# Optimization experiments

Hardware: AMD Instinct MI355X
Metric: run time of the kernel (lower is better)

Reference implementation:

```python
import jax, jax.numpy as jnp
import numpy as np

SCALE = 1.0 / np.sqrt(64.0)  # 1/sqrt(d), d = head_dim


def setup_inputs() -> dict:
    key = jax.random.key(0)
    kq, kk, kv = jax.random.split(key, 3)
    shape = (32, 2048, 64)  # [batch*num_heads, seq_len, head_dim]
    return {
        "queries": jax.random.normal(kq, shape, dtype=jnp.float32),
        "keys": jax.random.normal(kk, shape, dtype=jnp.float32),
        "values": jax.random.normal(kv, shape, dtype=jnp.float32),
    }


def reference(queries, keys, values):
    # scores = Q K^T / sqrt(d)   -> [n, q_len, kv_len]
    scores = jnp.einsum("nqd,nkd->nqk", queries, keys) * SCALE
    # masked_softmax with mask=None == plain softmax over last axis
    attn = jax.nn.softmax(scores, axis=-1)
    # dropout rate 0 / inference -> identity
    return jnp.einsum("nqk,nkd->nqd", attn, values)
```

## Files before the change

kernel.cpp:

```cpp
#include <hip/hip_runtime.h>
#include <hip/hip_bf16.h>

#define SEQ   2048
#define HDIM  64
#define KVT   64
#define NT    (SEQ / KVT)
#define M0    12.0f
#define QSC   0.18033688011112042f

typedef float f32x16 __attribute__((ext_vector_type(16)));
typedef short bf16x8 __attribute__((ext_vector_type(8)));
typedef short bf16x4 __attribute__((ext_vector_type(4)));

#define MFMA32(a, b, c) __builtin_amdgcn_mfma_f32_32x32x16_bf16(a, b, c, 0, 0, 0)

static __device__ __forceinline__ unsigned tobf(float x) {
    unsigned u = __builtin_bit_cast(unsigned, x);
    u += 0x7fff + ((u >> 16) & 1);
    return u >> 16;
}
static __device__ __forceinline__ unsigned pk2(float lo, float hi) {
    return (tobf(hi) << 16) | tobf(lo);
}
static __device__ __forceinline__ unsigned pkrn(float lo, float hi) {
    __hip_bfloat162 h = __float22bfloat162_rn(make_float2(lo, hi));
    unsigned r;
    __builtin_memcpy(&r, &h, sizeof(r));
    return r;
}

static __device__ __forceinline__ void gll16(const void* g, void* l) {
    __builtin_amdgcn_global_load_lds(
        (const __attribute__((address_space(1))) void*)g,
        (__attribute__((address_space(3))) void*)l, 16, 0, 0);
}

__global__ __launch_bounds__(256) void attn_prep(
    const float* __restrict__ K, const float* __restrict__ V,
    unsigned short* __restrict__ Kx, unsigned short* __restrict__ Vx)
{
    __shared__ unsigned short tile[64 * 64];
    const int bid = blockIdx.x;
    const int tid = threadIdx.x;
    if (bid < 4096) {
        const int id  = bid * 256 + tid;
        const int h   = id >> 15;
        const int key = (id >> 4) & 2047;
        const int f   = id & 15;
        const float4 kv = *(const float4*)(K + ((size_t)h * SEQ + key) * HDIM + f * 4);
        unsigned* dst = (unsigned*)(Kx + ((size_t)h * SEQ + key) * HDIM + ((f ^ (key & 15)) << 2));
        dst[0] = pk2(kv.x, kv.y);
        dst[1] = pk2(kv.z, kv.w);
    } else {
        const int b = bid - 4096;
        const int h = b >> 5, t = b & 31;
        const float* vb = V + ((size_t)h * SEQ + t * 64) * HDIM;
#pragma unroll
        for (int i = 0; i < 4; ++i) {
            const int idx = tid + i * 256;
            const int key = idx >> 4, f = idx & 15;
            float4 vv = *(const float4*)(vb + key * HDIM + f * 4);
            unsigned* d = (unsigned*)&tile[key * 64 + f * 4];
            d[0] = pk2(vv.x, vv.y);
            d[1] = pk2(vv.z, vv.w);
        }
        __syncthreads();
        unsigned short* vxb = Vx + ((size_t)h * SEQ + t * 64) * HDIM;
        const int dim = tid & 63;
#pragma unroll
        for (int j = 0; j < 4; ++j) {
            const int kb = (tid >> 6) + j * 4;
            const unsigned short s0 = tile[(kb * 4 + 0) * 64 + dim];
            const unsigned short s1 = tile[(kb * 4 + 1) * 64 + dim];
            const unsigned short s2 = tile[(kb * 4 + 2) * 64 + dim];
            const unsigned short s3 = tile[(kb * 4 + 3) * 64 + dim];
            unsigned* d = (unsigned*)&vxb[dim * 64 + ((kb ^ (dim & 15)) << 2)];
            d[0] = (unsigned)s0 | ((unsigned)s1 << 16);
            d[1] = (unsigned)s2 | ((unsigned)s3 << 16);
        }
    }
}

#define KBUF 8192

__global__ __launch_bounds__(256, 2) void attn_v5(
    const float* __restrict__ Q, const unsigned short* __restrict__ Kx,
    const unsigned short* __restrict__ Vx, float* __restrict__ O)
{
    __shared__ __align__(16) short Ks[2][KVT * HDIM];
    __shared__ __align__(16) short Vf[2][KVT * HDIM];
    __shared__ float Linv[128];

    const int tid  = threadIdx.x;
    const int lane = tid & 63;
    const int wid  = tid >> 6;
    const int n31  = lane & 31;
    const int hi   = lane >> 5;
    const int m15  = n31 & 15;

    const int id = blockIdx.x;
    const int n  = (id & 7) + 8 * (id >> 7);
    const int qt = (id >> 3) & 15;
    const int qb = qt * 128 + wid * 32;

    const float* Qb = Q + (size_t)n * SEQ * HDIM;
    const char* kg = (const char*)(Kx + (size_t)n * SEQ * HDIM);
    const char* vg = (const char*)(Vx + (size_t)n * SEQ * HDIM);

    int offKa_[4], offKb_[4];
#pragma unroll
    for (int c = 0; c < 4; ++c) {
        const int ba = (4 * c + 2 * hi) ^ m15;
        offKa_[c] = n31 * 128 + (ba << 3);
        offKb_[c] = n31 * 128 + ((ba ^ 1) << 3);
    }
    int offV_[2][4];
#pragma unroll
    for (int h = 0; h < 2; ++h)
#pragma unroll
    for (int i = 0; i < 4; ++i)
        offV_[h][i] = n31 * 128 + ((((8 * h + hi + 2 * i) ^ m15)) << 3);

    bf16x8 qf[4];
#pragma unroll
    for (int c = 0; c < 4; ++c) {
        const float* qp = Qb + (size_t)(qb + n31) * HDIM + c * 16 + hi * 8;
        float4 a = *(const float4*)qp;
        float4 b = *(const float4*)(qp + 4);
        union { unsigned w[4]; bf16x8 v; } u;
        u.w[0] = pkrn(a.x * QSC, a.y * QSC);
        u.w[1] = pkrn(a.z * QSC, a.w * QSC);
        u.w[2] = pkrn(b.x * QSC, b.y * QSC);
        u.w[3] = pkrn(b.z * QSC, b.w * QSC);
        qf[c] = u.v;
    }

    f32x16 NEGM;
#pragma unroll
    for (int r = 0; r < 16; ++r) NEGM[r] = -M0;

    f32x16 o0, o1;
#pragma unroll
    for (int r = 0; r < 16; ++r) { o0[r] = 0.f; o1[r] = 0.f; }
    float lac = 0.f;

    const int soff = wid * 1024 + lane * 16;

#define STAGE(GOFF, BUF)                                                         \
    {                                                                            \
        _Pragma("unroll")                                                        \
        for (int i = 0; i < 2; ++i) {                                            \
            gll16(kg + (GOFF) + soff + i * 4096,                                 \
                  (char*)Ks + (BUF) * KBUF + wid * 1024 + i * 4096);             \
            gll16(vg + (GOFF) + soff + i * 4096,                                 \
                  (char*)Vf + (BUF) * KBUF + wid * 1024 + i * 4096);             \
        }                                                                        \
    }

#define COMPUTE(BUF)                                                             \
    {                                                                            \
        _Pragma("unroll")                                                        \
        for (int h = 0; h < 2; ++h) {                                            \
            f32x16 s;                                                            \
            __builtin_amdgcn_s_setprio(1);                                       \
            {                                                                    \
                bf16x4 lo0 = *(const bf16x4*)((char*)Ks + (BUF) * KBUF + h * 4096 + offKa_[0]); \
                bf16x4 hh0 = *(const bf16x4*)((char*)Ks + (BUF) * KBUF + h * 4096 + offKb_[0]); \
                s = MFMA32(__builtin_shufflevector(lo0, hh0, 0, 1, 2, 3, 4, 5, 6, 7), qf[0], NEGM); \
            }                                                                    \
            _Pragma("unroll")                                                    \
            for (int c = 1; c < 4; ++c) {                                        \
                bf16x4 lo = *(const bf16x4*)((char*)Ks + (BUF) * KBUF + h * 4096 + offKa_[c]); \
                bf16x4 hh = *(const bf16x4*)((char*)Ks + (BUF) * KBUF + h * 4096 + offKb_[c]); \
                s = MFMA32(__builtin_shufflevector(lo, hh, 0, 1, 2, 3, 4, 5, 6, 7), qf[c], s); \
            }                                                                    \
            __builtin_amdgcn_s_setprio(0);                                       \
            float p[16];                                                         \
            _Pragma("unroll")                                                    \
            for (int r = 0; r < 16; ++r) p[r] = __builtin_amdgcn_exp2f(s[r]);    \
            {                                                                    \
                float a0 = (p[0] + p[1]) + (p[2] + p[3]);                        \
                float a1 = (p[4] + p[5]) + (p[6] + p[7]);                        \
                float a2 = (p[8] + p[9]) + (p[10] + p[11]);                      \
                float a3 = (p[12] + p[13]) + (p[14] + p[15]);                    \
                lac += (a0 + a1) + (a2 + a3);                                    \
            }                                                                    \
            union { unsigned w[4]; bf16x8 v; } pa1, pa2;                         \
            _Pragma("unroll")                                                    \
            for (int j = 0; j < 4; ++j) {                                        \
                pa1.w[j] = pkrn(p[2 * j], p[2 * j + 1]);                         \
                pa2.w[j] = pkrn(p[8 + 2 * j], p[8 + 2 * j + 1]);                 \
            }                                                                    \
            __builtin_amdgcn_s_setprio(1);                                       \
            _Pragma("unroll")                                                    \
            for (int dh = 0; dh < 2; ++dh) {                                     \
                bf16x4 u0 = *(const bf16x4*)((char*)Vf + (BUF) * KBUF + dh * 4096 + offV_[h][0]); \
                bf16x4 u1 = *(const bf16x4*)((char*)Vf + (BUF) * KBUF + dh * 4096 + offV_[h][1]); \
                bf16x4 u2 = *(const bf16x4*)((char*)Vf + (BUF) * KBUF + dh * 4096 + offV_[h][2]); \
                bf16x4 u3 = *(const bf16x4*)((char*)Vf + (BUF) * KBUF + dh * 4096 + offV_[h][3]); \
                bf16x8 v1 = __builtin_shufflevector(u0, u1, 0, 1, 2, 3, 4, 5, 6, 7); \
                bf16x8 v2 = __builtin_shufflevector(u2, u3, 0, 1, 2, 3, 4, 5, 6, 7); \
                if (dh == 0) { o0 = MFMA32(pa1.v, v1, o0); o0 = MFMA32(pa2.v, v2, o0); } \
                else         { o1 = MFMA32(pa1.v, v1, o1); o1 = MFMA32(pa2.v, v2, o1); } \
            }                                                                    \
            __builtin_amdgcn_s_setprio(0);                                       \
        }                                                                        \
    }

    STAGE(0, 0);
    asm volatile("s_waitcnt vmcnt(0)");
    __syncthreads();

    for (int t = 0; t < NT; t += 2) {
        const int g = t * 8192;
        STAGE(g + 8192, 1);
        COMPUTE(0);
        asm volatile("s_waitcnt vmcnt(0)");
        __syncthreads();
        if (t + 2 < NT) STAGE(g + 16384, 0);
        COMPUTE(1);
        asm volatile("s_waitcnt vmcnt(0)");
        __syncthreads();
    }

    float l = lac + __shfl_xor(lac, 32);
    if (hi == 0) Linv[wid * 32 + n31] = 1.f / l;
    __syncthreads();

    const size_t obase = ((size_t)n * SEQ + qb) * HDIM + n31;
#pragma unroll
    for (int r = 0; r < 16; ++r) {
        const int qrow = (r & 3) + 8 * (r >> 2) + 4 * hi;
        const float inv = Linv[wid * 32 + qrow];
        O[obase + (size_t)qrow * HDIM]      = o0[r] * inv;
        O[obase + (size_t)qrow * HDIM + 32] = o1[r] * inv;
    }
#undef STAGE
#undef COMPUTE
}

__global__ __launch_bounds__(256, 2) void attn_v3(
    const float* __restrict__ Q, const float* __restrict__ K,
    const float* __restrict__ V, float* __restrict__ O)
{
    __shared__ __align__(16) short Ks[2][KVT * HDIM];
    __shared__ __align__(16) short Vf[2][KVT * HDIM];
    __shared__ float Linv[128];

    const int tid  = threadIdx.x;
    const int lane = tid & 63;
    const int wid  = tid >> 6;
    const int n31  = lane & 31;
    const int hi   = lane >> 5;
    const int m15  = n31 & 15;

    const int id = blockIdx.x;
    const int n  = (id & 7) + 8 * (id >> 7);
    const int qt = (id >> 3) & 15;
    const int qb = qt * 128 + wid * 32;

    const float* Qb = Q + (size_t)n * SEQ * HDIM;
    const float* Kb = K + (size_t)n * SEQ * HDIM;
    const float* Vb = V + (size_t)n * SEQ * HDIM;

    const int sk_k0 = tid >> 4;
    const int sk_f  = tid & 15;
    const int sv_k  = tid & 63;
    const int sv_d0 = tid >> 6;

    bf16x8 qf[4];
#pragma unroll
    for (int c = 0; c < 4; ++c) {
        const float* qp = Qb + (size_t)(qb + n31) * HDIM + c * 16 + hi * 8;
        float4 a = *(const float4*)qp;
        float4 b = *(const float4*)(qp + 4);
        union { unsigned w[4]; bf16x8 v; } u;
        u.w[0] = pk2(a.x * QSC, a.y * QSC);
        u.w[1] = pk2(a.z * QSC, a.w * QSC);
        u.w[2] = pk2(b.x * QSC, b.y * QSC);
        u.w[3] = pk2(b.z * QSC, b.w * QSC);
        qf[c] = u.v;
    }

    f32x16 o0, o1;
#pragma unroll
    for (int r = 0; r < 16; ++r) { o0[r] = 0.f; o1[r] = 0.f; }
    float lac = 0.f;

    float4 kreg[4], vreg[4];

#define LOADT(T)                                                                \
    {                                                                           \
        const float* kp_ = Kb + (size_t)(T) * KVT * HDIM;                       \
        const float* vp_ = Vb + (size_t)(T) * KVT * HDIM;                       \
        _Pragma("unroll")                                                       \
        for (int i = 0; i < 4; ++i) {                                           \
            kreg[i] = *(const float4*)(kp_ + (sk_k0 + i * 16) * HDIM + sk_f * 4);\
            vreg[i] = *(const float4*)(vp_ + sv_k * HDIM + (sv_d0 + i * 4) * 4);\
        }                                                                       \
    }

#define WRITET(B)                                                               \
    {                                                                           \
        _Pragma("unroll")                                                       \
        for (int i = 0; i < 4; ++i) {                                           \
            const int k_ = sk_k0 + i * 16;                                      \
            union { unsigned w[2]; bf16x4 v; } u_;                              \
            u_.w[0] = pk2(kreg[i].x, kreg[i].y);                                \
            u_.w[1] = pk2(kreg[i].z, kreg[i].w);                                \
            *(bf16x4*)&Ks[B][k_ * 64 + ((sk_f ^ (k_ & 15)) << 2)] = u_.v;       \
            const int dq_ = sv_d0 + i * 4;                                      \
            const unsigned w0_ = pk2(vreg[i].x, vreg[i].y);                     \
            const unsigned w1_ = pk2(vreg[i].z, vreg[i].w);                     \
            _Pragma("unroll")                                                   \
            for (int r = 0; r < 4; ++r) {                                       \
                const int row_ = dq_ * 4 + r;                                   \
                const short val_ = (r == 0) ? (short)(w0_ & 0xffff)             \
                                 : (r == 1) ? (short)(w0_ >> 16)                \
                                 : (r == 2) ? (short)(w1_ & 0xffff)             \
                                            : (short)(w1_ >> 16);               \
                Vf[B][row_ * 64 + ((((sv_k >> 2) ^ (row_ & 15)) << 2) | (sv_k & 3))] = val_; \
            }                                                                   \
        }                                                                       \
    }

    LOADT(0);
    WRITET(0);
    __syncthreads();

    for (int t = 0; t < NT; ++t) {
        const int cur = t & 1;
        if (t + 1 < NT) LOADT(t + 1);

#pragma unroll
        for (int h = 0; h < 2; ++h) {
            const int key = h * 32 + n31;
            const short* Kp = &Ks[cur][key * 64];
            const int kx = key & 15;

            f32x16 s;
#pragma unroll
            for (int r = 0; r < 16; ++r) s[r] = -M0;

            __builtin_amdgcn_s_setprio(1);
#pragma unroll
            for (int c = 0; c < 4; ++c) {
                const int ba = 4 * c + 2 * hi;
                bf16x4 lo = *(const bf16x4*)&Kp[((ba    ) ^ kx) << 2];
                bf16x4 hh = *(const bf16x4*)&Kp[((ba + 1) ^ kx) << 2];
                bf16x8 kf = __builtin_shufflevector(lo, hh, 0, 1, 2, 3, 4, 5, 6, 7);
                s = MFMA32(kf, qf[c], s);
            }
            __builtin_amdgcn_s_setprio(0);

            float p[16];
#pragma unroll
            for (int r = 0; r < 16; ++r) p[r] = __builtin_amdgcn_exp2f(s[r]);
            {
                float a0 = (p[0] + p[1]) + (p[2] + p[3]);
                float a1 = (p[4] + p[5]) + (p[6] + p[7]);
                float a2 = (p[8] + p[9]) + (p[10] + p[11]);
                float a3 = (p[12] + p[13]) + (p[14] + p[15]);
                lac += (a0 + a1) + (a2 + a3);
            }

            union { unsigned w[4]; bf16x8 v; } pa1, pa2;
#pragma unroll
            for (int j = 0; j < 4; ++j) {
                pa1.w[j] = pk2(p[2 * j], p[2 * j + 1]);
                pa2.w[j] = pk2(p[8 + 2 * j], p[8 + 2 * j + 1]);
            }

            __builtin_amdgcn_s_setprio(1);
#pragma unroll
            for (int dh = 0; dh < 2; ++dh) {
                const short* Vp = &Vf[cur][(dh * 32 + n31) * 64];
                const int b0 = 8 * h + hi;
                bf16x4 u0 = *(const bf16x4*)&Vp[((b0    ) ^ m15) << 2];
                bf16x4 u1 = *(const bf16x4*)&Vp[((b0 + 2) ^ m15) << 2];
                bf16x4 u2 = *(const bf16x4*)&Vp[((b0 + 4) ^ m15) << 2];
                bf16x4 u3 = *(const bf16x4*)&Vp[((b0 + 6) ^ m15) << 2];
                bf16x8 v1 = __builtin_shufflevector(u0, u1, 0, 1, 2, 3, 4, 5, 6, 7);
                bf16x8 v2 = __builtin_shufflevector(u2, u3, 0, 1, 2, 3, 4, 5, 6, 7);
                if (dh == 0) { o0 = MFMA32(pa1.v, v1, o0); o0 = MFMA32(pa2.v, v2, o0); }
                else         { o1 = MFMA32(pa1.v, v1, o1); o1 = MFMA32(pa2.v, v2, o1); }
            }
            __builtin_amdgcn_s_setprio(0);
        }

        if (t + 1 < NT) WRITET((t + 1) & 1);
        __syncthreads();
    }

    float l = lac + __shfl_xor(lac, 32);
    if (hi == 0) Linv[wid * 32 + n31] = 1.f / l;
    __syncthreads();

    const size_t obase = ((size_t)n * SEQ + qb) * HDIM + n31;
#pragma unroll
    for (int r = 0; r < 16; ++r) {
        const int qrow = (r & 3) + 8 * (r >> 2) + 4 * hi;
        const float inv = Linv[wid * 32 + qrow];
        O[obase + (size_t)qrow * HDIM]      = o0[r] * inv;
        O[obase + (size_t)qrow * HDIM + 32] = o1[r] * inv;
    }
}

extern "C" void kernel_launch(void* const* d_in, const int* in_sizes, int n_in,
                              void* d_out, int out_size, void* d_ws, size_t ws_size,
                              hipStream_t stream) {
    const float* Q = (const float*)d_in[0];
    const float* K = (const float*)d_in[1];
    const float* V = (const float*)d_in[2];
    float* O = (float*)d_out;

    const size_t elems = (size_t)32 * SEQ * HDIM;
    const int nblk = (SEQ / 128) * 32;

    if (ws_size >= elems * 2 * 2) {
        unsigned short* Kx = (unsigned short*)d_ws;
        unsigned short* Vx = Kx + elems;
        attn_prep<<<4096 + 1024, 256, 0, stream>>>(K, V, Kx, Vx);
        attn_v5<<<nblk, 256, 0, stream>>>(Q, Kx, Vx, O);
    } else {
        attn_v3<<<nblk, 256, 0, stream>>>(Q, K, V, O);
    }
}
```

Measured before the change: 67.75 us.

## Split KV sequence across two wave groups per block and merge partial outputs

The attention kernel now launches 512 threads per block. Two halves of four waves each process disjoint halves of the key/value sequence for the same 128 query rows, using separate double-buffered shared memory regions. At the end, the second half writes its partial output accumulators and row sums to shared memory, and the first half adds them in, normalizes and stores. This doubles the waves available to hide latency and halves the serial KV loop per wave. The cost is more shared memory per block, a merge step and possibly lower block occupancy.

```diff
diff --git a/kernel.cpp b/kernel.cpp
--- a/kernel.cpp
+++ b/kernel.cpp
@@ -4,7 +4,6 @@
 #define SEQ   2048
 #define HDIM  64
 #define KVT   64
-#define NT    (SEQ / KVT)
 #define M0    12.0f
 #define QSC   0.18033688011112042f
 
@@ -82,18 +81,22 @@
 }
 
 #define KBUF 8192
-
-__global__ __launch_bounds__(256, 2) void attn_v5(
+#define HSTR 16384
+
+__global__ __launch_bounds__(512, 2) void attn_v6(
     const float* __restrict__ Q, const unsigned short* __restrict__ Kx,
     const unsigned short* __restrict__ Vx, float* __restrict__ O)
 {
-    __shared__ __align__(16) short Ks[2][KVT * HDIM];
-    __shared__ __align__(16) short Vf[2][KVT * HDIM];
+    __shared__ __align__(16) short Ks[2][2][KVT * HDIM];
+    __shared__ __align__(16) short Vf[2][2][KVT * HDIM];
+    __shared__ float L2[128];
     __shared__ float Linv[128];
 
     const int tid  = threadIdx.x;
     const int lane = tid & 63;
     const int wid  = tid >> 6;
+    const int qw   = wid & 3;
+    const int half = wid >> 2;
     const int n31  = lane & 31;
     const int hi   = lane >> 5;
     const int m15  = n31 & 15;
@@ -101,11 +104,13 @@
     const int id = blockIdx.x;
     const int n  = (id & 7) + 8 * (id >> 7);
     const int qt = (id >> 3) & 15;
-    const int qb = qt * 128 + wid * 32;
+    const int qb = qt * 128 + qw * 32;
 
     const float* Qb = Q + (size_t)n * SEQ * HDIM;
-    const char* kg = (const char*)(Kx + (size_t)n * SEQ * HDIM);
-    const char* vg = (const char*)(Vx + (size_t)n * SEQ * HDIM);
+    const char* kg = (const char*)(Kx + (size_t)n * SEQ * HDIM) + (size_t)half * 131072;
+    const char* vg = (const char*)(Vx + (size_t)n * SEQ * HDIM) + (size_t)half * 131072;
+    char* KsH = (char*)Ks + half * HSTR;
+    char* VfH = (char*)Vf + half * HSTR;
 
     int offKa_[4], offKb_[4];
 #pragma unroll
@@ -144,16 +149,16 @@
     for (int r = 0; r < 16; ++r) { o0[r] = 0.f; o1[r] = 0.f; }
     float lac = 0.f;
 
-    const int soff = wid * 1024 + lane * 16;
+    const int soff = qw * 1024 + lane * 16;
 
 #define STAGE(GOFF, BUF)                                                         \
     {                                                                            \
         _Pragma("unroll")                                                        \
         for (int i = 0; i < 2; ++i) {                                            \
             gll16(kg + (GOFF) + soff + i * 4096,                                 \
-                  (char*)Ks + (BUF) * KBUF + wid * 1024 + i * 4096);             \
+                  KsH + (BUF) * KBUF + qw * 1024 + i * 4096);                    \
             gll16(vg + (GOFF) + soff + i * 4096,                                 \
-                  (char*)Vf + (BUF) * KBUF + wid * 1024 + i * 4096);             \
+                  VfH + (BUF) * KBUF + qw * 1024 + i * 4096);                    \
         }                                                                        \
     }
 
@@ -164,14 +169,14 @@
             f32x16 s;                                                            \
             __builtin_amdgcn_s_setprio(1);                                       \
             {                                                                    \
-                bf16x4 lo0 = *(const bf16x4*)((char*)Ks + (BUF) * KBUF + h * 4096 + offKa_[0]); \
-                bf16x4 hh0 = *(const bf16x4*)((char*)Ks + (BUF) * KBUF + h * 4096 + offKb_[0]); \
+                bf16x4 lo0 = *(const bf16x4*)(KsH + (BUF) * KBUF + h * 4096 + offKa_[0]); \
+                bf16x4 hh0 = *(const bf16x4*)(KsH + (BUF) * KBUF + h * 4096 + offKb_[0]); \
                 s = MFMA32(__builtin_shufflevector(lo0, hh0, 0, 1, 2, 3, 4, 5, 6, 7), qf[0], NEGM); \
             }                                                                    \
             _Pragma("unroll")                                                    \
             for (int c = 1; c < 4; ++c) {                                        \
-                bf16x4 lo = *(const bf16x4*)((char*)Ks + (BUF) * KBUF + h * 4096 + offKa_[c]); \
-                bf16x4 hh = *(const bf16x4*)((char*)Ks + (BUF) * KBUF + h * 4096 + offKb_[c]); \
+                bf16x4 lo = *(const bf16x4*)(KsH + (BUF) * KBUF + h * 4096 + offKa_[c]); \
+                bf16x4 hh = *(const bf16x4*)(KsH + (BUF) * KBUF + h * 4096 + offKb_[c]); \
                 s = MFMA32(__builtin_shufflevector(lo, hh, 0, 1, 2, 3, 4, 5, 6, 7), qf[c], s); \
             }                                                                    \
             __builtin_amdgcn_s_setprio(0);                                       \
@@ -194,10 +199,10 @@
             __builtin_amdgcn_s_setprio(1);                                       \
             _Pragma("unroll")                                                    \
             for (int dh = 0; dh < 2; ++dh) {                                     \
-                bf16x4 u0 = *(const bf16x4*)((char*)Vf + (BUF) * KBUF + dh * 4096 + offV_[h][0]); \
-                bf16x4 u1 = *(const bf16x4*)((char*)Vf + (BUF) * KBUF + dh * 4096 + offV_[h][1]); \
-                bf16x4 u2 = *(const bf16x4*)((char*)Vf + (BUF) * KBUF + dh * 4096 + offV_[h][2]); \
-                bf16x4 u3 = *(const bf16x4*)((char*)Vf + (BUF) * KBUF + dh * 4096 + offV_[h][3]); \
+                bf16x4 u0 = *(const bf16x4*)(VfH + (BUF) * KBUF + dh * 4096 + offV_[h][0]); \
+                bf16x4 u1 = *(const bf16x4*)(VfH + (BUF) * KBUF + dh * 4096 + offV_[h][1]); \
+                bf16x4 u2 = *(const bf16x4*)(VfH + (BUF) * KBUF + dh * 4096 + offV_[h][2]); \
+                bf16x4 u3 = *(const bf16x4*)(VfH + (BUF) * KBUF + dh * 4096 + offV_[h][3]); \
                 bf16x8 v1 = __builtin_shufflevector(u0, u1, 0, 1, 2, 3, 4, 5, 6, 7); \
                 bf16x8 v2 = __builtin_shufflevector(u2, u3, 0, 1, 2, 3, 4, 5, 6, 7); \
                 if (dh == 0) { o0 = MFMA32(pa1.v, v1, o0); o0 = MFMA32(pa2.v, v2, o0); } \
@@ -211,29 +216,48 @@
     asm volatile("s_waitcnt vmcnt(0)");
     __syncthreads();
 
-    for (int t = 0; t < NT; t += 2) {
+    for (int t = 0; t < 16; t += 2) {
         const int g = t * 8192;
         STAGE(g + 8192, 1);
         COMPUTE(0);
         asm volatile("s_waitcnt vmcnt(0)");
         __syncthreads();
-        if (t + 2 < NT) STAGE(g + 16384, 0);
+        if (t + 2 < 16) STAGE(g + 16384, 0);
         COMPUTE(1);
         asm volatile("s_waitcnt vmcnt(0)");
         __syncthreads();
     }
 
     float l = lac + __shfl_xor(lac, 32);
-    if (hi == 0) Linv[wid * 32 + n31] = 1.f / l;
+
+    if (half == 1) {
+        if (hi == 0) L2[qw * 32 + n31] = l;
+        float* ob = (float*)((char*)Ks + qw * 8192) + lane * 32;
+        *(f32x16*)(ob)      = o0;
+        *(f32x16*)(ob + 16) = o1;
+    }
     __syncthreads();
 
-    const size_t obase = ((size_t)n * SEQ + qb) * HDIM + n31;
-#pragma unroll
-    for (int r = 0; r < 16; ++r) {
-        const int qrow = (r & 3) + 8 * (r >> 2) + 4 * hi;
-        const float inv = Linv[wid * 32 + qrow];
-        O[obase + (size_t)qrow * HDIM]      = o0[r] * inv;
-        O[obase + (size_t)qrow * HDIM + 32] = o1[r] * inv;
+    if (half == 0) {
+        const float* pb = (const float*)((char*)Ks + qw * 8192) + lane * 32;
+        f32x16 p0 = *(const f32x16*)(pb);
+        f32x16 p1 = *(const f32x16*)(pb + 16);
+#pragma unroll
+        for (int r = 0; r < 16; ++r) { o0[r] += p0[r]; o1[r] += p1[r]; }
+        l += L2[qw * 32 + n31];
+        if (hi == 0) Linv[qw * 32 + n31] = 1.f / l;
+    }
+    __syncthreads();
+
+    if (half == 0) {
+        const size_t obase = ((size_t)n * SEQ + qb) * HDIM + n31;
+#pragma unroll
+        for (int r = 0; r < 16; ++r) {
+            const int qrow = (r & 3) + 8 * (r >> 2) + 4 * hi;
+            const float inv = Linv[qw * 32 + qrow];
+            O[obase + (size_t)qrow * HDIM]      = o0[r] * inv;
+            O[obase + (size_t)qrow * HDIM + 32] = o1[r] * inv;
+        }
     }
 #undef STAGE
 #undef COMPUTE
@@ -243,9 +267,9 @@
     const float* __restrict__ Q, const float* __restrict__ K,
     const float* __restrict__ V, float* __restrict__ O)
 {
-    __shared__ __align__(16) short Ks[2][KVT * HDIM];
-    __shared__ __align__(16) short Vf[2][KVT * HDIM];
-    __shared__ float Linv[128];
+    __shared__ __align__(16) short Ksf[2][KVT * HDIM];
+    __shared__ __align__(16) short Vff[2][KVT * HDIM];
+    __shared__ float LinvF[128];
 
     const int tid  = threadIdx.x;
     const int lane = tid & 63;
@@ -308,7 +332,7 @@
             union { unsigned w[2]; bf16x4 v; } u_;                              \
             u_.w[0] = pk2(kreg[i].x, kreg[i].y);                                \
             u_.w[1] = pk2(kreg[i].z, kreg[i].w);                                \
-            *(bf16x4*)&Ks[B][k_ * 64 + ((sk_f ^ (k_ & 15)) << 2)] = u_.v;       \
+            *(bf16x4*)&Ksf[B][k_ * 64 + ((sk_f ^ (k_ & 15)) << 2)] = u_.v;      \
             const int dq_ = sv_d0 + i * 4;                                      \
             const unsigned w0_ = pk2(vreg[i].x, vreg[i].y);                     \
             const unsigned w1_ = pk2(vreg[i].z, vreg[i].w);                     \
@@ -319,7 +343,7 @@
                                  : (r == 1) ? (short)(w0_ >> 16)                \
                                  : (r == 2) ? (short)(w1_ & 0xffff)             \
                                             : (short)(w1_ >> 16);               \
-                Vf[B][row_ * 64 + ((((sv_k >> 2) ^ (row_ & 15)) << 2) | (sv_k & 3))] = val_; \
+                Vff[B][row_ * 64 + ((((sv_k >> 2) ^ (row_ & 15)) << 2) | (sv_k & 3))] = val_; \
             }                                                                   \
         }                                                                       \
     }
@@ -328,14 +352,14 @@
     WRITET(0);
     __syncthreads();
 
-    for (int t = 0; t < NT; ++t) {
+    for (int t = 0; t < SEQ / KVT; ++t) {
         const int cur = t & 1;
-        if (t + 1 < NT) LOADT(t + 1);
+        if (t + 1 < SEQ / KVT) LOADT(t + 1);
 
 #pragma unroll
         for (int h = 0; h < 2; ++h) {
             const int key = h * 32 + n31;
-            const short* Kp = &Ks[cur][key * 64];
+            const short* Kp = &Ksf[cur][key * 64];
             const int kx = key & 15;
 
             f32x16 s;
@@ -374,7 +398,7 @@
             __builtin_amdgcn_s_setprio(1);
 #pragma unroll
             for (int dh = 0; dh < 2; ++dh) {
-                const short* Vp = &Vf[cur][(dh * 32 + n31) * 64];
+                const short* Vp = &Vff[cur][(dh * 32 + n31) * 64];
                 const int b0 = 8 * h + hi;
                 bf16x4 u0 = *(const bf16x4*)&Vp[((b0    ) ^ m15) << 2];
                 bf16x4 u1 = *(const bf16x4*)&Vp[((b0 + 2) ^ m15) << 2];
@@ -388,19 +412,19 @@
             __builtin_amdgcn_s_setprio(0);
         }
 
-        if (t + 1 < NT) WRITET((t + 1) & 1);
+        if (t + 1 < SEQ / KVT) WRITET((t + 1) & 1);
         __syncthreads();
     }
 
     float l = lac + __shfl_xor(lac, 32);
-    if (hi == 0) Linv[wid * 32 + n31] = 1.f / l;
+    if (hi == 0) LinvF[wid * 32 + n31] = 1.f / l;
     __syncthreads();
 
     const size_t obase = ((size_t)n * SEQ + qb) * HDIM + n31;
 #pragma unroll
     for (int r = 0; r < 16; ++r) {
         const int qrow = (r & 3) + 8 * (r >> 2) + 4 * hi;
-        const float inv = Linv[wid * 32 + qrow];
+        const float inv = LinvF[wid * 32 + qrow];
         O[obase + (size_t)qrow * HDIM]      = o0[r] * inv;
         O[obase + (size_t)qrow * HDIM + 32] = o1[r] * inv;
     }
@@ -421,7 +445,7 @@
         unsigned short* Kx = (unsigned short*)d_ws;
         unsigned short* Vx = Kx + elems;
         attn_prep<<<4096 + 1024, 256, 0, stream>>>(K, V, Kx, Vx);
-        attn_v5<<<nblk, 256, 0, stream>>>(Q, Kx, Vx, O);
+        attn_v6<<<nblk, 512, 0, stream>>>(Q, Kx, Vx, O);
     } else {
         attn_v3<<<nblk, 256, 0, stream>>>(Q, K, V, O);
     }
```

Result: slower. 74.46 us (+9.9%).

## Split KV sequence across two blocks per query tile and add combine kernel

Applied to the files above, without the earlier changes.

Splits the key/value sequence into two halves, each processed by a separate block (1024 blocks, launch bounds raised to 4 per CU), writing unnormalized partial outputs in bf16 and row sums to workspace. A new combine kernel sums the partials and normalizes. This aims to raise occupancy and parallelism, at the cost of extra global traffic, an extra kernel launch, and bf16 rounding of partials. The small-workspace fallback now also writes to workspace.

```diff
diff --git a/kernel.cpp b/kernel.cpp
--- a/kernel.cpp
+++ b/kernel.cpp
@@ -5,6 +5,7 @@
 #define HDIM  64
 #define KVT   64
 #define NT    (SEQ / KVT)
+#define HT    16
 #define M0    12.0f
 #define QSC   0.18033688011112042f
 
@@ -27,6 +28,9 @@
     unsigned r;
     __builtin_memcpy(&r, &h, sizeof(r));
     return r;
+}
+static __device__ __forceinline__ float bf2f(unsigned short u) {
+    return __builtin_bit_cast(float, ((unsigned)u) << 16);
 }
 
 static __device__ __forceinline__ void gll16(const void* g, void* l) {
@@ -83,13 +87,13 @@
 
 #define KBUF 8192
 
-__global__ __launch_bounds__(256, 2) void attn_v5(
+__global__ __launch_bounds__(256, 4) void attn_v7(
     const float* __restrict__ Q, const unsigned short* __restrict__ Kx,
-    const unsigned short* __restrict__ Vx, float* __restrict__ O)
+    const unsigned short* __restrict__ Vx,
+    unsigned short* __restrict__ Pp, float* __restrict__ Lp)
 {
     __shared__ __align__(16) short Ks[2][KVT * HDIM];
     __shared__ __align__(16) short Vf[2][KVT * HDIM];
-    __shared__ float Linv[128];
 
     const int tid  = threadIdx.x;
     const int lane = tid & 63;
@@ -98,14 +102,16 @@
     const int hi   = lane >> 5;
     const int m15  = n31 & 15;
 
-    const int id = blockIdx.x;
-    const int n  = (id & 7) + 8 * (id >> 7);
-    const int qt = (id >> 3) & 15;
+    const int id    = blockIdx.x;
+    const int id9   = id & 511;
+    const int split = id >> 9;
+    const int n  = (id9 & 7) + 8 * (id9 >> 7);
+    const int qt = (id9 >> 3) & 15;
     const int qb = qt * 128 + wid * 32;
 
     const float* Qb = Q + (size_t)n * SEQ * HDIM;
-    const char* kg = (const char*)(Kx + (size_t)n * SEQ * HDIM);
-    const char* vg = (const char*)(Vx + (size_t)n * SEQ * HDIM);
+    const char* kg = (const char*)(Kx + (size_t)n * SEQ * HDIM) + (size_t)split * (HT * KBUF);
+    const char* vg = (const char*)(Vx + (size_t)n * SEQ * HDIM) + (size_t)split * (HT * KBUF);
 
     int offKa_[4], offKb_[4];
 #pragma unroll
@@ -211,6 +217,178 @@
     asm volatile("s_waitcnt vmcnt(0)");
     __syncthreads();
 
+    for (int t = 0; t < HT; t += 2) {
+        const int g = t * 8192;
+        STAGE(g + 8192, 1);
+        COMPUTE(0);
+        asm volatile("s_waitcnt vmcnt(0)");
+        __syncthreads();
+        if (t + 2 < HT) STAGE(g + 16384, 0);
+        COMPUTE(1);
+        asm volatile("s_waitcnt vmcnt(0)");
+        __syncthreads();
+    }
+
+    float l = lac + __shfl_xor(lac, 32);
+    if (hi == 0) Lp[split * 65536 + n * SEQ + qb + n31] = l;
+
+    unsigned short* pb = Pp + (size_t)split * 4194304
+                       + ((size_t)n * SEQ + qb) * HDIM + n31;
+#pragma unroll
+    for (int r = 0; r < 16; ++r) {
+        const int qrow = (r & 3) + 8 * (r >> 2) + 4 * hi;
+        pb[(size_t)qrow * HDIM]      = (unsigned short)tobf(o0[r]);
+        pb[(size_t)qrow * HDIM + 32] = (unsigned short)tobf(o1[r]);
+    }
+#undef STAGE
+#undef COMPUTE
+}
+
+__global__ __launch_bounds__(256) void attn_comb(
+    const unsigned short* __restrict__ Pp, const float* __restrict__ Lp,
+    float* __restrict__ O)
+{
+    const int f = blockIdx.x * 256 + threadIdx.x;
+    const int qidx = f >> 4;
+    const float inv = 1.f / (Lp[qidx] + Lp[65536 + qidx]);
+    const ushort4 a = *(const ushort4*)(Pp + (size_t)f * 4);
+    const ushort4 b = *(const ushort4*)(Pp + 4194304 + (size_t)f * 4);
+    float4 o;
+    o.x = (bf2f(a.x) + bf2f(b.x)) * inv;
+    o.y = (bf2f(a.y) + bf2f(b.y)) * inv;
+    o.z = (bf2f(a.z) + bf2f(b.z)) * inv;
+    o.w = (bf2f(a.w) + bf2f(b.w)) * inv;
+    reinterpret_cast<float4*>(O)[f] = o;
+}
+
+__global__ __launch_bounds__(256, 2) void attn_v5(
+    const float* __restrict__ Q, const unsigned short* __restrict__ Kx,
+    const unsigned short* __restrict__ Vx, float* __restrict__ O)
+{
+    __shared__ __align__(16) short Ks[2][KVT * HDIM];
+    __shared__ __align__(16) short Vf[2][KVT * HDIM];
+    __shared__ float Linv[128];
+
+    const int tid  = threadIdx.x;
+    const int lane = tid & 63;
+    const int wid  = tid >> 6;
+    const int n31  = lane & 31;
+    const int hi   = lane >> 5;
+    const int m15  = n31 & 15;
+
+    const int id = blockIdx.x;
+    const int n  = (id & 7) + 8 * (id >> 7);
+    const int qt = (id >> 3) & 15;
+    const int qb = qt * 128 + wid * 32;
+
+    const float* Qb = Q + (size_t)n * SEQ * HDIM;
+    const char* kg = (const char*)(Kx + (size_t)n * SEQ * HDIM);
+    const char* vg = (const char*)(Vx + (size_t)n * SEQ * HDIM);
+
+    int offKa_[4], offKb_[4];
+#pragma unroll
+    for (int c = 0; c < 4; ++c) {
+        const int ba = (4 * c + 2 * hi) ^ m15;
+        offKa_[c] = n31 * 128 + (ba << 3);
+        offKb_[c] = n31 * 128 + ((ba ^ 1) << 3);
+    }
+    int offV_[2][4];
+#pragma unroll
+    for (int h = 0; h < 2; ++h)
+#pragma unroll
+    for (int i = 0; i < 4; ++i)
+        offV_[h][i] = n31 * 128 + ((((8 * h + hi + 2 * i) ^ m15)) << 3);
+
+    bf16x8 qf[4];
+#pragma unroll
+    for (int c = 0; c < 4; ++c) {
+        const float* qp = Qb + (size_t)(qb + n31) * HDIM + c * 16 + hi * 8;
+        float4 a = *(const float4*)qp;
+        float4 b = *(const float4*)(qp + 4);
+        union { unsigned w[4]; bf16x8 v; } u;
+        u.w[0] = pkrn(a.x * QSC, a.y * QSC);
+        u.w[1] = pkrn(a.z * QSC, a.w * QSC);
+        u.w[2] = pkrn(b.x * QSC, b.y * QSC);
+        u.w[3] = pkrn(b.z * QSC, b.w * QSC);
+        qf[c] = u.v;
+    }
+
+    f32x16 NEGM;
+#pragma unroll
+    for (int r = 0; r < 16; ++r) NEGM[r] = -M0;
+
+    f32x16 o0, o1;
+#pragma unroll
+    for (int r = 0; r < 16; ++r) { o0[r] = 0.f; o1[r] = 0.f; }
+    float lac = 0.f;
+
+    const int soff = wid * 1024 + lane * 16;
+
+#define STAGE(GOFF, BUF)                                                         \
+    {                                                                            \
+        _Pragma("unroll")                                                        \
+        for (int i = 0; i < 2; ++i) {                                            \
+            gll16(kg + (GOFF) + soff + i * 4096,                                 \
+                  (char*)Ks + (BUF) * KBUF + wid * 1024 + i * 4096);             \
+            gll16(vg + (GOFF) + soff + i * 4096,                                 \
+                  (char*)Vf + (BUF) * KBUF + wid * 1024 + i * 4096);             \
+        }                                                                        \
+    }
+
+#define COMPUTE(BUF)                                                             \
+    {                                                                            \
+        _Pragma("unroll")                                                        \
+        for (int h = 0; h < 2; ++h) {                                            \
+            f32x16 s;                                                            \
+            __builtin_amdgcn_s_setprio(1);                                       \
+            {                                                                    \
+                bf16x4 lo0 = *(const bf16x4*)((char*)Ks + (BUF) * KBUF + h * 4096 + offKa_[0]); \
+                bf16x4 hh0 = *(const bf16x4*)((char*)Ks + (BUF) * KBUF + h * 4096 + offKb_[0]); \
+                s = MFMA32(__builtin_shufflevector(lo0, hh0, 0, 1, 2, 3, 4, 5, 6, 7), qf[0], NEGM); \
+            }                                                                    \
+            _Pragma("unroll")                                                    \
+            for (int c = 1; c < 4; ++c) {                                        \
+                bf16x4 lo = *(const bf16x4*)((char*)Ks + (BUF) * KBUF + h * 4096 + offKa_[c]); \
+                bf16x4 hh = *(const bf16x4*)((char*)Ks + (BUF) * KBUF + h * 4096 + offKb_[c]); \
+                s = MFMA32(__builtin_shufflevector(lo, hh, 0, 1, 2, 3, 4, 5, 6, 7), qf[c], s); \
+            }                                                                    \
+            __builtin_amdgcn_s_setprio(0);                                       \
+            float p[16];                                                         \
+            _Pragma("unroll")                                                    \
+            for (int r = 0; r < 16; ++r) p[r] = __builtin_amdgcn_exp2f(s[r]);    \
+            {                                                                    \
+                float a0 = (p[0] + p[1]) + (p[2] + p[3]);                        \
+                float a1 = (p[4] + p[5]) + (p[6] + p[7]);                        \
+                float a2 = (p[8] + p[9]) + (p[10] + p[11]);                      \
+                float a3 = (p[12] + p[13]) + (p[14] + p[15]);                    \
+                lac += (a0 + a1) + (a2 + a3);                                    \
+            }                                                                    \
+            union { unsigned w[4]; bf16x8 v; } pa1, pa2;                         \
+            _Pragma("unroll")                                                    \
+            for (int j = 0; j < 4; ++j) {                                        \
+                pa1.w[j] = pkrn(p[2 * j], p[2 * j + 1]);                         \
+                pa2.w[j] = pkrn(p[8 + 2 * j], p[8 + 2 * j + 1]);                 \
+            }                                                                    \
+            __builtin_amdgcn_s_setprio(1);                                       \
+            _Pragma("unroll")                                                    \
+            for (int dh = 0; dh < 2; ++dh) {                                     \
+                bf16x4 u0 = *(const bf16x4*)((char*)Vf + (BUF) * KBUF + dh * 4096 + offV_[h][0]); \
+                bf16x4 u1 = *(const bf16x4*)((char*)Vf + (BUF) * KBUF + dh * 4096 + offV_[h][1]); \
+                bf16x4 u2 = *(const bf16x4*)((char*)Vf + (BUF) * KBUF + dh * 4096 + offV_[h][2]); \
+                bf16x4 u3 = *(const bf16x4*)((char*)Vf + (BUF) * KBUF + dh * 4096 + offV_[h][3]); \
+                bf16x8 v1 = __builtin_shufflevector(u0, u1, 0, 1, 2, 3, 4, 5, 6, 7); \
+                bf16x8 v2 = __builtin_shufflevector(u2, u3, 0, 1, 2, 3, 4, 5, 6, 7); \
+                if (dh == 0) { o0 = MFMA32(pa1.v, v1, o0); o0 = MFMA32(pa2.v, v2, o0); } \
+                else         { o1 = MFMA32(pa1.v, v1, o1); o1 = MFMA32(pa2.v, v2, o1); } \
+            }                                                                    \
+            __builtin_amdgcn_s_setprio(0);                                       \
+        }                                                                        \
+    }
+
+    STAGE(0, 0);
+    asm volatile("s_waitcnt vmcnt(0)");
+    __syncthreads();
+
     for (int t = 0; t < NT; t += 2) {
         const int g = t * 8192;
         STAGE(g + 8192, 1);
@@ -239,173 +417,6 @@
 #undef COMPUTE
 }
 
-__global__ __launch_bounds__(256, 2) void attn_v3(
-    const float* __restrict__ Q, const float* __restrict__ K,
-    const float* __restrict__ V, float* __restrict__ O)
-{
-    __shared__ __align__(16) short Ks[2][KVT * HDIM];
-    __shared__ __align__(16) short Vf[2][KVT * HDIM];
-    __shared__ float Linv[128];
-
-    const int tid  = threadIdx.x;
-    const int lane = tid & 63;
-    const int wid  = tid >> 6;
-    const int n31  = lane & 31;
-    const int hi   = lane >> 5;
-    const int m15  = n31 & 15;
-
-    const int id = blockIdx.x;
-    const int n  = (id & 7) + 8 * (id >> 7);
-    const int qt = (id >> 3) & 15;
-    const int qb = qt * 128 + wid * 32;
-
-    const float* Qb = Q + (size_t)n * SEQ * HDIM;
-    const float* Kb = K + (size_t)n * SEQ * HDIM;
-    const float* Vb = V + (size_t)n * SEQ * HDIM;
-
-    const int sk_k0 = tid >> 4;
-    const int sk_f  = tid & 15;
-    const int sv_k  = tid & 63;
-    const int sv_d0 = tid >> 6;
-
-    bf16x8 qf[4];
-#pragma unroll
-    for (int c = 0; c < 4; ++c) {
-        const float* qp = Qb + (size_t)(qb + n31) * HDIM + c * 16 + hi * 8;
-        float4 a = *(const float4*)qp;
-        float4 b = *(const float4*)(qp + 4);
-        union { unsigned w[4]; bf16x8 v; } u;
-        u.w[0] = pk2(a.x * QSC, a.y * QSC);
-        u.w[1] = pk2(a.z * QSC, a.w * QSC);
-        u.w[2] = pk2(b.x * QSC, b.y * QSC);
-        u.w[3] = pk2(b.z * QSC, b.w * QSC);
-        qf[c] = u.v;
-    }
-
-    f32x16 o0, o1;
-#pragma unroll
-    for (int r = 0; r < 16; ++r) { o0[r] = 0.f; o1[r] = 0.f; }
-    float lac = 0.f;
-
-    float4 kreg[4], vreg[4];
-
-#define LOADT(T)                                                                \
-    {                                                                           \
-        const float* kp_ = Kb + (size_t)(T) * KVT * HDIM;                       \
-        const float* vp_ = Vb + (size_t)(T) * KVT * HDIM;                       \
-        _Pragma("unroll")                                                       \
-        for (int i = 0; i < 4; ++i) {                                           \
-            kreg[i] = *(const float4*)(kp_ + (sk_k0 + i * 16) * HDIM + sk_f * 4);\
-            vreg[i] = *(const float4*)(vp_ + sv_k * HDIM + (sv_d0 + i * 4) * 4);\
-        }                                                                       \
-    }
-
-#define WRITET(B)                                                               \
-    {                                                                           \
-        _Pragma("unroll")                                                       \
-        for (int i = 0; i < 4; ++i) {                                           \
-            const int k_ = sk_k0 + i * 16;                                      \
-            union { unsigned w[2]; bf16x4 v; } u_;                              \
-            u_.w[0] = pk2(kreg[i].x, kreg[i].y);                                \
-            u_.w[1] = pk2(kreg[i].z, kreg[i].w);                                \
-            *(bf16x4*)&Ks[B][k_ * 64 + ((sk_f ^ (k_ & 15)) << 2)] = u_.v;       \
-            const int dq_ = sv_d0 + i * 4;                                      \
-            const unsigned w0_ = pk2(vreg[i].x, vreg[i].y);                     \
-            const unsigned w1_ = pk2(vreg[i].z, vreg[i].w);                     \
-            _Pragma("unroll")                                                   \
-            for (int r = 0; r < 4; ++r) {                                       \
-                const int row_ = dq_ * 4 + r;                                   \
-                const short val_ = (r == 0) ? (short)(w0_ & 0xffff)             \
-                                 : (r == 1) ? (short)(w0_ >> 16)                \
-                                 : (r == 2) ? (short)(w1_ & 0xffff)             \
-                                            : (short)(w1_ >> 16);               \
-                Vf[B][row_ * 64 + ((((sv_k >> 2) ^ (row_ & 15)) << 2) | (sv_k & 3))] = val_; \
-            }                                                                   \
-        }                                                                       \
-    }
-
-    LOADT(0);
-    WRITET(0);
-    __syncthreads();
-
-    for (int t = 0; t < NT; ++t) {
-        const int cur = t & 1;
-        if (t + 1 < NT) LOADT(t + 1);
-
-#pragma unroll
-        for (int h = 0; h < 2; ++h) {
-            const int key = h * 32 + n31;
-            const short* Kp = &Ks[cur][key * 64];
-            const int kx = key & 15;
-
-            f32x16 s;
-#pragma unroll
-            for (int r = 0; r < 16; ++r) s[r] = -M0;
-
-            __builtin_amdgcn_s_setprio(1);
-#pragma unroll
-            for (int c = 0; c < 4; ++c) {
-                const int ba = 4 * c + 2 * hi;
-                bf16x4 lo = *(const bf16x4*)&Kp[((ba    ) ^ kx) << 2];
-                bf16x4 hh = *(const bf16x4*)&Kp[((ba + 1) ^ kx) << 2];
-                bf16x8 kf = __builtin_shufflevector(lo, hh, 0, 1, 2, 3, 4, 5, 6, 7);
-                s = MFMA32(kf, qf[c], s);
-            }
-            __builtin_amdgcn_s_setprio(0);
-
-            float p[16];
-#pragma unroll
-            for (int r = 0; r < 16; ++r) p[r] = __builtin_amdgcn_exp2f(s[r]);
-            {
-                float a0 = (p[0] + p[1]) + (p[2] + p[3]);
-                float a1 = (p[4] + p[5]) + (p[6] + p[7]);
-                float a2 = (p[8] + p[9]) + (p[10] + p[11]);
-                float a3 = (p[12] + p[13]) + (p[14] + p[15]);
-                lac += (a0 + a1) + (a2 + a3);
-            }
-
-            union { unsigned w[4]; bf16x8 v; } pa1, pa2;
-#pragma unroll
-            for (int j = 0; j < 4; ++j) {
-                pa1.w[j] = pk2(p[2 * j], p[2 * j + 1]);
-                pa2.w[j] = pk2(p[8 + 2 * j], p[8 + 2 * j + 1]);
-            }
-
-            __builtin_amdgcn_s_setprio(1);
-#pragma unroll
-            for (int dh = 0; dh < 2; ++dh) {
-                const short* Vp = &Vf[cur][(dh * 32 + n31) * 64];
-                const int b0 = 8 * h + hi;
-                bf16x4 u0 = *(const bf16x4*)&Vp[((b0    ) ^ m15) << 2];
-                bf16x4 u1 = *(const bf16x4*)&Vp[((b0 + 2) ^ m15) << 2];
-                bf16x4 u2 = *(const bf16x4*)&Vp[((b0 + 4) ^ m15) << 2];
-                bf16x4 u3 = *(const bf16x4*)&Vp[((b0 + 6) ^ m15) << 2];
-                bf16x8 v1 = __builtin_shufflevector(u0, u1, 0, 1, 2, 3, 4, 5, 6, 7);
-                bf16x8 v2 = __builtin_shufflevector(u2, u3, 0, 1, 2, 3, 4, 5, 6, 7);
-                if (dh == 0) { o0 = MFMA32(pa1.v, v1, o0); o0 = MFMA32(pa2.v, v2, o0); }
-                else         { o1 = MFMA32(pa1.v, v1, o1); o1 = MFMA32(pa2.v, v2, o1); }
-            }
-            __builtin_amdgcn_s_setprio(0);
-        }
-
-        if (t + 1 < NT) WRITET((t + 1) & 1);
-        __syncthreads();
-    }
-
-    float l = lac + __shfl_xor(lac, 32);
-    if (hi == 0) Linv[wid * 32 + n31] = 1.f / l;
-    __syncthreads();
-
-    const size_t obase = ((size_t)n * SEQ + qb) * HDIM + n31;
-#pragma unroll
-    for (int r = 0; r < 16; ++r) {
-        const int qrow = (r & 3) + 8 * (r >> 2) + 4 * hi;
-        const float inv = Linv[wid * 32 + qrow];
-        O[obase + (size_t)qrow * HDIM]      = o0[r] * inv;
-        O[obase + (size_t)qrow * HDIM + 32] = o1[r] * inv;
-    }
-}
-
 extern "C" void kernel_launch(void* const* d_in, const int* in_sizes, int n_in,
                               void* d_out, int out_size, void* d_ws, size_t ws_size,
                               hipStream_t stream) {
@@ -417,12 +428,21 @@
     const size_t elems = (size_t)32 * SEQ * HDIM;
     const int nblk = (SEQ / 128) * 32;
 
-    if (ws_size >= elems * 2 * 2) {
-        unsigned short* Kx = (unsigned short*)d_ws;
-        unsigned short* Vx = Kx + elems;
+    char* ws = (char*)d_ws;
+    unsigned short* Kx = (unsigned short*)ws;
+    unsigned short* Vx = (unsigned short*)(ws + 8388608);
+    unsigned short* Pp = (unsigned short*)(ws + 16777216);
+    float*          Lp = (float*)(ws + 33554432);
+
+    if (ws_size >= 34078720) {
+        attn_prep<<<4096 + 1024, 256, 0, stream>>>(K, V, Kx, Vx);
+        attn_v7<<<2 * nblk, 256, 0, stream>>>(Q, Kx, Vx, Pp, Lp);
+        attn_comb<<<4096, 256, 0, stream>>>(Pp, Lp, O);
+    } else if (ws_size >= elems * 2 * 2) {
         attn_prep<<<4096 + 1024, 256, 0, stream>>>(K, V, Kx, Vx);
         attn_v5<<<nblk, 256, 0, stream>>>(Q, Kx, Vx, O);
     } else {
-        attn_v3<<<nblk, 256, 0, stream>>>(Q, K, V, O);
-    }
-}
+        attn_prep<<<4096 + 1024, 256, 0, stream>>>(K, V, Kx, Vx);
+        attn_v5<<<nblk, 256, 0, stream>>>(Q, Kx, Vx, O);
+    }
+}
```

Measured after the change: 107.9 us. +59.2%, slower.
